# Optimization experiments

Hardware: AMD Instinct MI355X
Metric: run time of the kernel (lower is better)

The kernel has to match this reference:

```python
import jax, jax.numpy as jnp
import numpy as np

H = 64  # hidden_size


def _lstm_layer(xs, Wih, Whh, bih, bhh):
    # xs: (S, B, in_dim). PyTorch gate order: i, f, g, o.
    S, B, _ = xs.shape
    b = bih + bhh  # (4H,)
    # Precompute input projections for all timesteps (one big GEMM)
    x_proj = jnp.einsum('sbi,gi->sbg', xs, Wih) + b  # (S, B, 4H)

    def step(carry, xp_t):
        h, c = carry
        gates = xp_t + h @ Whh.T  # (B, 4H)
        i, f, g, o = jnp.split(gates, 4, axis=-1)
        i = jax.nn.sigmoid(i)
        f = jax.nn.sigmoid(f)
        g = jnp.tanh(g)
        o = jax.nn.sigmoid(o)
        c = f * c + i * g
        h = o * jnp.tanh(c)
        return (h, c), h

    h0 = jnp.zeros((B, H), dtype=xs.dtype)
    c0 = jnp.zeros((B, H), dtype=xs.dtype)
    _, ys = jax.lax.scan(step, (h0, c0), x_proj)
    return ys  # (S, B, H)


def setup_inputs() -> dict:
    key = jax.random.key(0)
    ks = jax.random.split(key, 16)
    scale = 1.0 / np.sqrt(H)  # PyTorch uniform(-1/sqrt(H), 1/sqrt(H)) scale

    def u(k, shape):
        return jax.random.uniform(k, shape, jnp.float32, -scale, scale)

    inp = {
        'x': jax.random.normal(ks[0], (512, 2048, 4), dtype=jnp.float32),
        # layer 0: input_size=4
        'Wih0': u(ks[1], (4 * H, 4)), 'Whh0': u(ks[2], (4 * H, H)),
        'bih0': u(ks[3], (4 * H,)), 'bhh0': u(ks[4], (4 * H,)),
        # layers 1,2: input_size=H
        'Wih1': u(ks[5], (4 * H, H)), 'Whh1': u(ks[6], (4 * H, H)),
        'bih1': u(ks[7], (4 * H,)), 'bhh1': u(ks[8], (4 * H,)),
        'Wih2': u(ks[9], (4 * H, H)), 'Whh2': u(ks[10], (4 * H, H)),
        'bih2': u(ks[11], (4 * H,)), 'bhh2': u(ks[12], (4 * H,)),
        # fc: Linear(64, 2)
        'fc_w': u(ks[13], (2, H)), 'fc_b': u(ks[14], (2,)),
    }
    return inp


def reference(x, Wih0, Whh0, bih0, bhh0, Wih1, Whh1, bih1, bhh1,
              Wih2, Whh2, bih2, bhh2, fc_w, fc_b):
    xs = jnp.transpose(x, (1, 0, 2))  # (S, B, 4) -- x.permute(1,0,2)
    h = _lstm_layer(xs, Wih0, Whh0, bih0, bhh0)
    h = _lstm_layer(h, Wih1, Whh1, bih1, bhh1)
    h = _lstm_layer(h, Wih2, Whh2, bih2, bhh2)
    last = h[-1]  # (B, H) -- out[-1]
    return last @ fc_w.T + fc_b  # (B, 2)
```

## Files before the change

kernel.cpp:

```cpp
#include <hip/hip_runtime.h>

#define SS 2048
#define BATCH 512
#define NB 2
#define NT 512

typedef float f2 __attribute__((ext_vector_type(2)));

__device__ __forceinline__ float fast_rcp(float a) { return __builtin_amdgcn_rcpf(a); }
__device__ __forceinline__ float fast_exp2(float a) { return __builtin_amdgcn_exp2f(a); }

__device__ __forceinline__ f2 pk_fma(f2 a, f2 b, f2 c) {
  return __builtin_elementwise_fma(a, b, c);
}
__device__ __forceinline__ f2 pk_mul(f2 a, f2 b) { return a * b; }

template <int CTRL>
__device__ __forceinline__ float dpp_add(float v) {
  const int sh = __builtin_amdgcn_update_dpp(0, __float_as_int(v), CTRL, 0xf, 0xf, true);
  return v + __int_as_float(sh);
}

template <int CTRL>
__device__ __forceinline__ float dpp_mov(float v) {
  return __int_as_float(__builtin_amdgcn_update_dpp(0, __float_as_int(v), CTRL, 0xf, 0xf, true));
}

__device__ __forceinline__ void ld8(const float* p, f2 (&hv)[4]) {
  const float4 A = *(const float4*)p;
  const float4 B = *(const float4*)(p + 4);
  hv[0] = f2{A.x, A.y}; hv[1] = f2{A.z, A.w};
  hv[2] = f2{B.x, B.y}; hv[3] = f2{B.z, B.w};
}

__device__ __forceinline__ void mv8p_first(const f2 (&w)[4][4], const f2 (&hv)[4],
                                           f2 (&acc)[4]) {
#pragma unroll
  for (int g = 0; g < 4; ++g) {
    acc[g] = pk_mul(w[g][0], hv[0]);
#pragma unroll
    for (int k = 1; k < 4; ++k) acc[g] = pk_fma(w[g][k], hv[k], acc[g]);
  }
}
__device__ __forceinline__ void mv8p(const f2 (&w)[4][4], const f2 (&hv)[4],
                                     f2 (&acc)[4]) {
#pragma unroll
  for (int g = 0; g < 4; ++g) {
#pragma unroll
    for (int k = 0; k < 4; ++k) acc[g] = pk_fma(w[g][k], hv[k], acc[g]);
  }
}

__device__ __forceinline__ float redsel(f2 (&a2)[4], bool kb0, bool kb1) {
  float a[4];
#pragma unroll
  for (int g = 0; g < 4; ++g) a[g] = a2[g].x + a2[g].y;
#pragma unroll
  for (int g = 0; g < 4; ++g) {
    a[g] = dpp_add<0xB1>(a[g]);
    a[g] = dpp_add<0x4E>(a[g]);
  }
  const float s01 = kb0 ? a[1] : a[0];
  const float s23 = kb0 ? a[3] : a[2];
  float s = kb1 ? s23 : s01;
  s = dpp_add<0x141>(s);
  return s;
}

__device__ __forceinline__ float gate_finish(float pre, float kact, float aact,
                                             float bact, float& c) {
  const float e = fast_exp2(kact * pre);
  const float r = fast_rcp(1.0f + e);
  const float a = fmaf(aact, r, bact);
  const float vi = dpp_mov<0x00>(a);
  const float vf = dpp_mov<0x55>(a);
  const float vg = dpp_mov<0xAA>(a);
  const float vo = dpp_mov<0xFF>(a);
  c = fmaf(vf, c, vi * vg);
  const float te = fast_exp2(2.8853900817779268f * c);
  const float tr = fast_rcp(1.0f + te);
  const float t = vo * tr;
  return fmaf(-2.0f, t, vo);
}

template <int CUR, int NXT>
__device__ __forceinline__ void lstm_step(
    float (&hb)[2][3][NB][64],
    const f2 (&whh0)[4][4], const f2 (&wih1)[4][4],
    const f2 (&whh1)[4][4], const f2 (&wih2)[4][4],
    const f2 (&whh2)[4][4],
    const float (&wi0l)[4],
    float b0l, float b1l, float b2l,
    float kact, float aact, float bact,
    float (&c0)[NB], float (&c1)[NB], float (&c2)[NB],
    const float (&xin)[NB][4], int j, int k0,
    bool kb0, bool kb1, bool wr,
    bool act0, bool act1, bool act2) {
  f2 p0[NB][4], p1[NB][4], p2[NB][4];
#pragma unroll
  for (int b = 0; b < NB; ++b) {
    f2 hv0[4], hv1[4], hv2[4];
    ld8(&hb[CUR][0][b][k0], hv0);
    ld8(&hb[CUR][1][b][k0], hv1);
    ld8(&hb[CUR][2][b][k0], hv2);
    mv8p_first(whh0, hv0, p0[b]);
    mv8p_first(wih1, hv0, p1[b]);
    mv8p      (whh1, hv1, p1[b]);
    mv8p_first(wih2, hv1, p2[b]);
    mv8p      (whh2, hv2, p2[b]);
  }
#pragma unroll
  for (int b = 0; b < NB; ++b) {
    float s0 = redsel(p0[b], kb0, kb1);
    float d = b0l;
#pragma unroll
    for (int f2i = 0; f2i < 4; ++f2i) d = fmaf(wi0l[f2i], xin[b][f2i], d);
    float cc0 = c0[b];
    const float h0 = gate_finish(s0 + d, kact, aact, bact, cc0);
    if (act0) { c0[b] = cc0; if (wr) hb[NXT][0][b][j] = h0; }
    float cc1 = c1[b];
    const float h1 = gate_finish(redsel(p1[b], kb0, kb1) + b1l, kact, aact, bact, cc1);
    if (act1) { c1[b] = cc1; if (wr) hb[NXT][1][b][j] = h1; }
    float cc2 = c2[b];
    const float h2 = gate_finish(redsel(p2[b], kb0, kb1) + b2l, kact, aact, bact, cc2);
    if (act2) { c2[b] = cc2; if (wr) hb[NXT][2][b][j] = h2; }
  }
  __syncthreads();
}

__global__ void __launch_bounds__(NT, 2)
lstm3_kernel(const float* __restrict__ x,
             const float* __restrict__ Wih0, const float* __restrict__ Whh0,
             const float* __restrict__ bih0, const float* __restrict__ bhh0,
             const float* __restrict__ Wih1, const float* __restrict__ Whh1,
             const float* __restrict__ bih1, const float* __restrict__ bhh1,
             const float* __restrict__ Wih2, const float* __restrict__ Whh2,
             const float* __restrict__ bih2, const float* __restrict__ bhh2,
             const float* __restrict__ fcw, const float* __restrict__ fcb,
             float* __restrict__ out) {
  __shared__ float hb[2][3][NB][64];
  const int tid = threadIdx.x;
  const int j = tid >> 3;
  const int ko = tid & 7;
  const int k0 = ko << 3;
  const int bbase = blockIdx.x * NB;
  const int gl = (ko & 4) ? (3 - (ko & 3)) : (ko & 3);
  const bool kb0 = (gl & 1) != 0;
  const bool kb1 = (gl & 2) != 0;
  const bool wr = (ko == 0);

  f2 whh0[4][4], wih1[4][4], whh1[4][4], wih2[4][4], whh2[4][4];
#pragma unroll
  for (int g = 0; g < 4; ++g) {
    const int r = (g << 6) + j;
    const int ro = (r << 6) + k0;
#define LDW(dst, srcp)                                            \
    {                                                             \
      const float4 A = *(const float4*)&(srcp)[ro];               \
      const float4 B = *(const float4*)&(srcp)[ro + 4];           \
      dst[g][0] = f2{A.x, A.y}; dst[g][1] = f2{A.z, A.w};         \
      dst[g][2] = f2{B.x, B.y}; dst[g][3] = f2{B.z, B.w};         \
    }
    LDW(whh0, Whh0)
    LDW(wih1, Wih1)
    LDW(whh1, Whh1)
    LDW(wih2, Wih2)
    LDW(whh2, Whh2)
#undef LDW
  }

  const int rl = (gl << 6) + j;
  const float b0l = bih0[rl] + bhh0[rl];
  const float b1l = bih1[rl] + bhh1[rl];
  const float b2l = bih2[rl] + bhh2[rl];
  float wi0l[4];
  {
    const float4 w0 = *(const float4*)&Wih0[rl * 4];
    wi0l[0] = w0.x; wi0l[1] = w0.y; wi0l[2] = w0.z; wi0l[3] = w0.w;
  }
  const bool isg = (gl == 2);
  const float kact = isg ? 2.8853900817779268f : -1.4426950408889634f;
  const float aact = isg ? -2.0f : 1.0f;
  const float bact = isg ? 1.0f : 0.0f;

  float c0[NB], c1[NB], c2[NB];
#pragma unroll
  for (int b = 0; b < NB; ++b) { c0[b] = 0.f; c1[b] = 0.f; c2[b] = 0.f; }

  {
    float* p = &hb[0][0][0][0];
    for (int i = tid; i < 2 * 3 * NB * 64; i += NT) p[i] = 0.f;
  }

  float xc[NB][4], xn[NB][4];
#pragma unroll
  for (int b = 0; b < NB; ++b) {
    const float4 v = *(const float4*)&x[(size_t)(bbase + b) * SS * 4];
    xc[b][0] = v.x; xc[b][1] = v.y; xc[b][2] = v.z; xc[b][3] = v.w;
  }
  __syncthreads();

#pragma unroll 1
  for (int t = 0; t < SS + 2; t += 2) {
    {
      const int i1 = (t + 1 < SS) ? (t + 1) : (SS - 1);
#pragma unroll
      for (int b = 0; b < NB; ++b) {
        const float4 v = *(const float4*)&x[((size_t)(bbase + b) * SS + i1) * 4];
        xn[b][0] = v.x; xn[b][1] = v.y; xn[b][2] = v.z; xn[b][3] = v.w;
      }
    }
    lstm_step<0, 1>(hb, whh0, wih1, whh1, wih2, whh2, wi0l, b0l, b1l, b2l,
                    kact, aact, bact, c0, c1, c2, xc, j, k0, kb0, kb1, wr,
                    t < SS, (t >= 1) && (t <= SS),
                    t >= 2);
    {
      const int i2 = (t + 2 < SS) ? (t + 2) : (SS - 1);
#pragma unroll
      for (int b = 0; b < NB; ++b) {
        const float4 v = *(const float4*)&x[((size_t)(bbase + b) * SS + i2) * 4];
        xc[b][0] = v.x; xc[b][1] = v.y; xc[b][2] = v.z; xc[b][3] = v.w;
      }
    }
    lstm_step<1, 0>(hb, whh0, wih1, whh1, wih2, whh2, wi0l, b0l, b1l, b2l,
                    kact, aact, bact, c0, c1, c2, xn, j, k0, kb0, kb1, wr,
                    t + 1 < SS, t + 1 <= SS,
                    t + 1 >= 2);
  }
  __syncthreads();

  if (tid < NB * 2) {
    const int b = tid >> 1, o = tid & 1;
    float s = fcb[o];
#pragma unroll
    for (int jj = 0; jj < 64; ++jj)
      s = fmaf(fcw[o * 64 + jj], hb[0][2][b][jj], s);
    out[(bbase + b) * 2 + o] = s;
  }
}

extern "C" void kernel_launch(void* const* d_in, const int* in_sizes, int n_in,
                              void* d_out, int out_size, void* d_ws, size_t ws_size,
                              hipStream_t stream) {
  const float* x    = (const float*)d_in[0];
  const float* Wih0 = (const float*)d_in[1];
  const float* Whh0 = (const float*)d_in[2];
  const float* bih0 = (const float*)d_in[3];
  const float* bhh0 = (const float*)d_in[4];
  const float* Wih1 = (const float*)d_in[5];
  const float* Whh1 = (const float*)d_in[6];
  const float* bih1 = (const float*)d_in[7];
  const float* bhh1 = (const float*)d_in[8];
  const float* Wih2 = (const float*)d_in[9];
  const float* Whh2 = (const float*)d_in[10];
  const float* bih2 = (const float*)d_in[11];
  const float* bhh2 = (const float*)d_in[12];
  const float* fcw  = (const float*)d_in[13];
  const float* fcb  = (const float*)d_in[14];
  float* out = (float*)d_out;

  lstm3_kernel<<<dim3(BATCH / NB), dim3(NT), 0, stream>>>(
      x, Wih0, Whh0, bih0, bhh0, Wih1, Whh1, bih1, bhh1,
      Wih2, Whh2, bih2, bhh2, fcw, fcb, out);
}
```

Before: 3.468 ms.

## Split batch rows across lane halves in gate epilogue and use raw LDS barrier

Each 8-lane group used to finish both batch rows redundantly. It now exchanges partial sums across the two 4-lane halves so that each half finishes the gates, cell update and tanh for one batch row. This halves the transcendental and epilogue work per lane and shrinks the per-lane cell state to scalars, at the cost of extra selects and a dpp exchange. It also replaces __syncthreads with an inline s_waitcnt lgkmcnt(0) plus s_barrier, which skips the compiler's more conservative fence.

```diff
diff --git a/kernel.cpp b/kernel.cpp
--- a/kernel.cpp
+++ b/kernel.cpp
@@ -20,10 +20,13 @@
   const int sh = __builtin_amdgcn_update_dpp(0, __float_as_int(v), CTRL, 0xf, 0xf, true);
   return v + __int_as_float(sh);
 }
-
 template <int CTRL>
 __device__ __forceinline__ float dpp_mov(float v) {
   return __int_as_float(__builtin_amdgcn_update_dpp(0, __float_as_int(v), CTRL, 0xf, 0xf, true));
+}
+
+__device__ __forceinline__ void lds_barrier() {
+  asm volatile("s_waitcnt lgkmcnt(0)\n\ts_barrier" ::: "memory");
 }
 
 __device__ __forceinline__ void ld8(const float* p, f2 (&hv)[4]) {
@@ -51,32 +54,39 @@
   }
 }
 
-__device__ __forceinline__ float redsel(f2 (&a2)[4], bool kb0, bool kb1) {
-  float a[4];
-#pragma unroll
-  for (int g = 0; g < 4; ++g) a[g] = a2[g].x + a2[g].y;
+__device__ __forceinline__ float redsel2(const f2 (&A)[4], const f2 (&B)[4],
+                                         bool kb0, bool kb1, bool bsel) {
+  float a[4], b[4];
+#pragma unroll
+  for (int g = 0; g < 4; ++g) { a[g] = A[g].x + A[g].y; b[g] = B[g].x + B[g].y; }
 #pragma unroll
   for (int g = 0; g < 4; ++g) {
     a[g] = dpp_add<0xB1>(a[g]);
     a[g] = dpp_add<0x4E>(a[g]);
-  }
-  const float s01 = kb0 ? a[1] : a[0];
-  const float s23 = kb0 ? a[3] : a[2];
-  float s = kb1 ? s23 : s01;
-  s = dpp_add<0x141>(s);
-  return s;
-}
-
-__device__ __forceinline__ float gate_finish(float pre, float kact, float aact,
-                                             float bact, float& c) {
+    b[g] = dpp_add<0xB1>(b[g]);
+    b[g] = dpp_add<0x4E>(b[g]);
+  }
+  const float t0 = kb1 ? (kb0 ? a[3] : a[2]) : (kb0 ? a[1] : a[0]);
+  const float t1 = kb1 ? (kb0 ? b[3] : b[2]) : (kb0 ? b[1] : b[0]);
+  const float send = bsel ? t0 : t1;
+  const float recv = dpp_mov<0x141>(send);
+  const float own  = bsel ? t1 : t0;
+  return own + recv;
+}
+
+__device__ __forceinline__ float gate_finish2(float pre, float kact, float aact,
+                                              float bact, float& c, bool bsel) {
   const float e = fast_exp2(kact * pre);
   const float r = fast_rcp(1.0f + e);
   const float a = fmaf(aact, r, bact);
-  const float vi = dpp_mov<0x00>(a);
-  const float vf = dpp_mov<0x55>(a);
-  const float vg = dpp_mov<0xAA>(a);
-  const float vo = dpp_mov<0xFF>(a);
-  c = fmaf(vf, c, vi * vg);
+  const float u0 = dpp_mov<0x00>(a);
+  const float u1 = dpp_mov<0x55>(a);
+  const float u2 = dpp_mov<0xAA>(a);
+  const float u3 = dpp_mov<0xFF>(a);
+  const float prod = bsel ? (u3 * u1) : (u0 * u2);
+  const float vf   = bsel ? u2 : u1;
+  const float vo   = bsel ? u0 : u3;
+  c = fmaf(vf, c, prod);
   const float te = fast_exp2(2.8853900817779268f * c);
   const float tr = fast_rcp(1.0f + te);
   const float t = vo * tr;
@@ -92,9 +102,9 @@
     const float (&wi0l)[4],
     float b0l, float b1l, float b2l,
     float kact, float aact, float bact,
-    float (&c0)[NB], float (&c1)[NB], float (&c2)[NB],
-    const float (&xin)[NB][4], int j, int k0,
-    bool kb0, bool kb1, bool wr,
+    float& c0, float& c1, float& c2,
+    const float (&xin)[NB][4], int j, int k0, int bi,
+    bool kb0, bool kb1, bool bsel, bool wq,
     bool act0, bool act1, bool act2) {
   f2 p0[NB][4], p1[NB][4], p2[NB][4];
 #pragma unroll
@@ -109,23 +119,29 @@
     mv8p_first(wih2, hv1, p2[b]);
     mv8p      (whh2, hv2, p2[b]);
   }
-#pragma unroll
-  for (int b = 0; b < NB; ++b) {
-    float s0 = redsel(p0[b], kb0, kb1);
+  {
+    const float s = redsel2(p0[0], p0[1], kb0, kb1, bsel);
     float d = b0l;
 #pragma unroll
-    for (int f2i = 0; f2i < 4; ++f2i) d = fmaf(wi0l[f2i], xin[b][f2i], d);
-    float cc0 = c0[b];
-    const float h0 = gate_finish(s0 + d, kact, aact, bact, cc0);
-    if (act0) { c0[b] = cc0; if (wr) hb[NXT][0][b][j] = h0; }
-    float cc1 = c1[b];
-    const float h1 = gate_finish(redsel(p1[b], kb0, kb1) + b1l, kact, aact, bact, cc1);
-    if (act1) { c1[b] = cc1; if (wr) hb[NXT][1][b][j] = h1; }
-    float cc2 = c2[b];
-    const float h2 = gate_finish(redsel(p2[b], kb0, kb1) + b2l, kact, aact, bact, cc2);
-    if (act2) { c2[b] = cc2; if (wr) hb[NXT][2][b][j] = h2; }
-  }
-  __syncthreads();
+    for (int f = 0; f < 4; ++f)
+      d = fmaf(wi0l[f], bsel ? xin[1][f] : xin[0][f], d);
+    float cc = c0;
+    const float h = gate_finish2(s + d, kact, aact, bact, cc, bsel);
+    if (act0) { c0 = cc; if (wq) hb[NXT][0][bi][j] = h; }
+  }
+  {
+    const float s = redsel2(p1[0], p1[1], kb0, kb1, bsel);
+    float cc = c1;
+    const float h = gate_finish2(s + b1l, kact, aact, bact, cc, bsel);
+    if (act1) { c1 = cc; if (wq) hb[NXT][1][bi][j] = h; }
+  }
+  {
+    const float s = redsel2(p2[0], p2[1], kb0, kb1, bsel);
+    float cc = c2;
+    const float h = gate_finish2(s + b2l, kact, aact, bact, cc, bsel);
+    if (act2) { c2 = cc; if (wq) hb[NXT][2][bi][j] = h; }
+  }
+  lds_barrier();
 }
 
 __global__ void __launch_bounds__(NT, 2)
@@ -147,7 +163,9 @@
   const int gl = (ko & 4) ? (3 - (ko & 3)) : (ko & 3);
   const bool kb0 = (gl & 1) != 0;
   const bool kb1 = (gl & 2) != 0;
-  const bool wr = (ko == 0);
+  const int  bi   = (ko >> 2) & 1;
+  const bool bsel = bi != 0;
+  const bool wq   = (ko & 3) == 0;
 
   f2 whh0[4][4], wih1[4][4], whh1[4][4], wih2[4][4], whh2[4][4];
 #pragma unroll
@@ -183,9 +201,7 @@
   const float aact = isg ? -2.0f : 1.0f;
   const float bact = isg ? 1.0f : 0.0f;
 
-  float c0[NB], c1[NB], c2[NB];
-#pragma unroll
-  for (int b = 0; b < NB; ++b) { c0[b] = 0.f; c1[b] = 0.f; c2[b] = 0.f; }
+  float c0 = 0.f, c1 = 0.f, c2 = 0.f;
 
   {
     float* p = &hb[0][0][0][0];
@@ -211,7 +227,8 @@
       }
     }
     lstm_step<0, 1>(hb, whh0, wih1, whh1, wih2, whh2, wi0l, b0l, b1l, b2l,
-                    kact, aact, bact, c0, c1, c2, xc, j, k0, kb0, kb1, wr,
+                    kact, aact, bact, c0, c1, c2, xc, j, k0, bi,
+                    kb0, kb1, bsel, wq,
                     t < SS, (t >= 1) && (t <= SS),
                     t >= 2);
     {
@@ -223,7 +240,8 @@
       }
     }
     lstm_step<1, 0>(hb, whh0, wih1, whh1, wih2, whh2, wi0l, b0l, b1l, b2l,
-                    kact, aact, bact, c0, c1, c2, xn, j, k0, kb0, kb1, wr,
+                    kact, aact, bact, c0, c1, c2, xn, j, k0, bi,
+                    kb0, kb1, bsel, wq,
                     t + 1 < SS, t + 1 <= SS,
                     t + 1 >= 2);
   }
```

After: 3.093 ms. -10.8%, faster.
